# Kernel tuning notes

Measured on AMD Instinct MI355X. Metric: run time of the kernel, lower is better.

Reference implementation:

```python
import jax, jax.numpy as jnp
import numpy as np

D_MODEL = 512
N_HEADS = 16
D_HEAD = D_MODEL // N_HEADS


def _relative_shift(pos_score):
    # pos_score: [B, H, T, T]  (Transformer-XL shift trick)
    B, H, T1, T2 = pos_score.shape
    padded = jnp.pad(pos_score, ((0, 0), (0, 0), (0, 0), (1, 0)))  # [B,H,T1,T2+1]
    padded = padded.reshape(B, H, T2 + 1, T1)
    return padded[:, :, 1:].reshape(B, H, T1, T2)


def setup_inputs() -> dict:
    key = jax.random.key(0)
    ks = jax.random.split(key, 12)
    B, T, D = 4, 1024, D_MODEL
    s = 1.0 / np.sqrt(D)
    return {
        "q": jax.random.normal(ks[0], (B, T, D), jnp.float32),
        "k": jax.random.normal(ks[1], (B, T, D), jnp.float32),
        "v": jax.random.normal(ks[2], (B, T, D), jnp.float32),
        "pos_embedding": jax.random.normal(ks[3], (B, T, D), jnp.float32),
        "Wq": jax.random.normal(ks[4], (D, D), jnp.float32) * s,
        "bq": jnp.zeros((D,), jnp.float32),
        "Wp": jax.random.normal(ks[5], (D, D), jnp.float32) * s,
        "Wf": jax.random.normal(ks[6], (D, D), jnp.float32) * s,
        "bf": jnp.zeros((D,), jnp.float32),
        "u_bias": jax.random.normal(ks[7], (N_HEADS, D_HEAD), jnp.float32) * s,
        "v_bias": jax.random.normal(ks[8], (N_HEADS, D_HEAD), jnp.float32) * s,
    }


def reference(q, k, v, pos_embedding, Wq, bq, Wp, Wf, bf, u_bias, v_bias):
    B, T, D = q.shape
    H, Dh = N_HEADS, D_HEAD
    sqrt_dim = jnp.asarray(np.sqrt(D_MODEL), q.dtype)
    # NOTE: original module uses linear_q for q, k AND v (faithful to source)
    qh = (q @ Wq + bq).reshape(B, T, H, Dh)            # [B,T,H,Dh]
    kh = (k @ Wq + bq).reshape(B, T, H, Dh)
    vh = (v @ Wq + bq).reshape(B, T, H, Dh)
    ph = (pos_embedding @ Wp).reshape(B, T, H, Dh)     # no bias

    content_score = jnp.einsum('bthd,bshd->bhts', qh + u_bias, kh)
    pos_score = jnp.einsum('bthd,bshd->bhts', qh + v_bias, ph)
    pos_score = _relative_shift(pos_score)

    score = (content_score + pos_score) / sqrt_dim     # [B,H,T,T]
    attn = jax.nn.softmax(score, axis=-1)              # dropout identity in eval
    context = jnp.einsum('bhts,bshd->bthd', attn, vh).reshape(B, T, D)
    return context @ Wf + bf
```

## Files before the change

### kernel.cpp

```cpp
#include <hip/hip_runtime.h>
#include <hip/hip_bf16.h>

typedef __bf16 bf16;
typedef bf16 bf16x8 __attribute__((ext_vector_type(8)));
typedef bf16 bf16x4 __attribute__((ext_vector_type(4)));
typedef float f32x4 __attribute__((ext_vector_type(4)));

#define SCALE_LOG2 0.06376237f


__global__ __launch_bounds__(256) void prep_kernel(
    const float* __restrict__ Wq, const float* __restrict__ Wp, const float* __restrict__ Wf,
    bf16* __restrict__ WqT, bf16* __restrict__ WpT, bf16* __restrict__ WfT)
{
  const int tid = threadIdx.x;
  __shared__ bf16 t[64][72];
  const int m = blockIdx.x >> 6;
  const int tb = blockIdx.x & 63;
  const int tr = tb >> 3, tc = tb & 7;
  const float* W = (m == 0) ? Wq : (m == 1) ? Wp : Wf;
  bf16*        O = (m == 0) ? WqT : (m == 1) ? WpT : WfT;
  const int r = tid >> 2, cg = tid & 3;
  {
    const float* src = W + (size_t)(tr * 64 + r) * 512 + tc * 64 + cg * 16;
    f32x4 a = *(const f32x4*)src, b2 = *(const f32x4*)(src + 4);
    f32x4 c = *(const f32x4*)(src + 8), d = *(const f32x4*)(src + 12);
    bf16x8 lo, hi;
#pragma unroll
    for (int j = 0; j < 4; j++) { lo[j] = (bf16)a[j]; lo[4 + j] = (bf16)b2[j]; hi[j] = (bf16)c[j]; hi[4 + j] = (bf16)d[j]; }
    *(bf16x8*)(&t[r][cg * 16])     = lo;
    *(bf16x8*)(&t[r][cg * 16 + 8]) = hi;
  }
  __syncthreads();
  bf16x8 o0, o1;
#pragma unroll
  for (int j = 0; j < 8; j++) { o0[j] = t[cg * 16 + j][r]; o1[j] = t[cg * 16 + 8 + j][r]; }
  bf16* dst = O + (size_t)(tc * 64 + r) * 512 + tr * 64 + cg * 16;
  *(bf16x8*)dst = o0;
  *(bf16x8*)(dst + 8) = o1;
}

__global__ __launch_bounds__(256) void proj_gemm(
    const float* __restrict__ q, const float* __restrict__ k, const float* __restrict__ v,
    const float* __restrict__ pos,
    const bf16* __restrict__ WqT, const bf16* __restrict__ WpT, const float* __restrict__ bq,
    bf16* __restrict__ qh, bf16* __restrict__ kh, bf16* __restrict__ vT, bf16* __restrict__ phx)
{
  __shared__ float Asf[128 * 68];
  __shared__ bf16  Bs[128 * 72];
  const int tid = threadIdx.x;
  const int wave = tid >> 6, lane = tid & 63, quad = lane >> 4, ln = lane & 15;
  const int tn = blockIdx.x & 3;
  const int tm = blockIdx.x >> 2;
  const int kind = tm >> 5;
  const int rr0 = (tm & 31) * 128;
  const float* X = (kind == 0) ? q : (kind == 1) ? k : (kind == 2) ? v : pos;
  const bf16* WT = ((kind < 3) ? WqT : WpT) + (size_t)tn * 128 * 512;
  const int qn_ = (wave & 1) * 64;
  const int qr_ = (wave >> 1) * 64;
  const int srow = tid >> 2, scg = tid & 3;

  f32x4 acc[4][4] = {};

  for (int kk = 0; kk < 8; kk++) {
    const int k0 = kk * 64;
    {
      const float* p0 = X + (size_t)(rr0 + srow) * 512 + k0 + scg * 16;
      const float* p1 = X + (size_t)(rr0 + srow + 64) * 512 + k0 + scg * 16;
#pragma unroll
      for (int u = 0; u < 4; u++) {
        *(f32x4*)(Asf + srow * 68 + scg * 16 + u * 4)        = *(const f32x4*)(p0 + u * 4);
        *(f32x4*)(Asf + (srow + 64) * 68 + scg * 16 + u * 4) = *(const f32x4*)(p1 + u * 4);
      }
      const bf16* w0 = WT + (size_t)srow * 512 + k0 + scg * 16;
      const bf16* w1 = WT + (size_t)(srow + 64) * 512 + k0 + scg * 16;
      *(bf16x8*)(Bs + srow * 72 + scg * 16)            = *(const bf16x8*)w0;
      *(bf16x8*)(Bs + srow * 72 + scg * 16 + 8)        = *(const bf16x8*)(w0 + 8);
      *(bf16x8*)(Bs + (srow + 64) * 72 + scg * 16)     = *(const bf16x8*)w1;
      *(bf16x8*)(Bs + (srow + 64) * 72 + scg * 16 + 8) = *(const bf16x8*)(w1 + 8);
    }
    __syncthreads();
#pragma unroll
    for (int ks = 0; ks < 2; ks++) {
      bf16x8 wf[4], xf[4];
#pragma unroll
      for (int i = 0; i < 4; i++) {
        wf[i] = *(const bf16x8*)(Bs + (qn_ + i * 16 + ln) * 72 + ks * 32 + quad * 8);
        f32x4 lo = *(const f32x4*)(Asf + (qr_ + i * 16 + ln) * 68 + ks * 32 + quad * 8);
        f32x4 hi = *(const f32x4*)(Asf + (qr_ + i * 16 + ln) * 68 + ks * 32 + quad * 8 + 4);
        bf16x8 t;
#pragma unroll
        for (int j = 0; j < 4; j++) { t[j] = (bf16)lo[j]; t[4 + j] = (bf16)hi[j]; }
        xf[i] = t;
      }
#pragma unroll
      for (int i = 0; i < 4; i++)
#pragma unroll
        for (int j = 0; j < 4; j++)
          acc[i][j] = __builtin_amdgcn_mfma_f32_16x16x32_bf16(wf[i], xf[j], acc[i][j], 0, 0, 0);
    }
    __syncthreads();
  }

#pragma unroll
  for (int i = 0; i < 4; i++) {
    const int nn0 = tn * 128 + qn_ + i * 16 + quad * 4;
    const int dd0 = nn0 & 31, hh = nn0 >> 5;
    f32x4 b4 = {0.f, 0.f, 0.f, 0.f};
    if (kind < 3) b4 = *(const f32x4*)(bq + nn0);
#pragma unroll
    for (int j = 0; j < 4; j++) {
      const int rr = rr0 + qr_ + j * 16 + ln;
      const int bb = rr >> 10, tt = rr & 1023;
      const size_t base = (size_t)(bb * 16 + hh);
      bf16x4 pk;
#pragma unroll
      for (int r = 0; r < 4; r++) pk[r] = (bf16)(acc[i][j][r] + b4[r]);
      if (kind == 0)      *(bf16x4*)(qh + (base * 1024 + tt) * 32 + dd0) = pk;
      else if (kind == 1) *(bf16x4*)(kh + (base * 1024 + tt) * 32 + dd0) = pk;
      else if (kind == 2) {
#pragma unroll
        for (int r = 0; r < 4; r++) vT[(base * 32 + dd0 + r) * 1024 + tt] = pk[r];
      } else {
        *(bf16x4*)(phx + (base * 2048 + tt) * 32 + dd0) = pk;
        if (tt <= 1021) *(bf16x4*)(phx + (base * 2048 + tt + 1025) * 32 + dd0) = pk;
        if (tt == 1023) {
          bf16x4 zz = {};
          *(bf16x4*)(phx + (base * 2048 + 1024) * 32 + dd0) = zz;
          *(bf16x4*)(phx + (base * 2048 + 2047) * 32 + dd0) = zz;
        }
      }
    }
  }
}

__global__ __launch_bounds__(256, 4) void attn_kernel(
    const bf16* __restrict__ qh, const bf16* __restrict__ kh,
    const bf16* __restrict__ vT, const bf16* __restrict__ phx,
    const float* __restrict__ u_bias, const float* __restrict__ v_bias,
    bf16* __restrict__ ctx)
{
  __shared__ float fs[4 * 16 * 84];
  __shared__ bf16  pb[4 * 16 * 72];

  const int tid = threadIdx.x;
  const int wave = tid >> 6, lane = tid & 63, quad = lane >> 4, ln = lane & 15;
  const int wg = blockIdx.x;
  const int bh = wg & 63, tq = wg >> 6;
  const int h = bh & 15, b = bh >> 4;
  const int t0 = tq * 64;
  const bf16* qh_h  = qh  + (size_t)bh * 1024 * 32;
  const bf16* kh_h  = kh  + (size_t)bh * 1024 * 32;
  const bf16* vT_h  = vT  + (size_t)bh * 32 * 1024;
  const bf16* phx_h = phx + (size_t)bh * 2048 * 32;

  float* fsw = fs + wave * 16 * 84;
  bf16*  pbw = pb + wave * 16 * 72;

  bf16x8 qu, qva, qvn;
  {
    const int t = t0 + wave * 16 + ln;
    bf16x8 q0 = *(const bf16x8*)(qh_h + (size_t)t * 32 + quad * 8);
    bf16x8 q1 = *(const bf16x8*)(qh_h + (size_t)(t + 1) * 32 + quad * 8);
    const float* ubp = u_bias + h * 32 + quad * 8;
    const float* vbp = v_bias + h * 32 + quad * 8;
#pragma unroll
    for (int j = 0; j < 8; j++) {
      qu[j]  = (bf16)(((float)q0[j] + ubp[j]) * SCALE_LOG2);
      qva[j] = (bf16)(((float)q0[j] + vbp[j]) * SCALE_LOG2);
      qvn[j] = (bf16)(((float)q1[j] + vbp[j]) * SCALE_LOG2);
    }
  }

  f32x4 O0 = {0.f, 0.f, 0.f, 0.f}, O1 = {0.f, 0.f, 0.f, 0.f};
  float l_lane = 0.0f;
  const f32x4 zf = {0.f, 0.f, 0.f, 0.f};

#pragma unroll 2
  for (int si = 0; si < 16; si++) {
    const int s0 = si * 64;
    const int jb0 = s0 - t0 + 960 + (3 - wave) * 16;

#pragma unroll
    for (int i = 0; i < 5; i++) {
      bf16x8 pbf = *(const bf16x8*)(phx_h + (size_t)(jb0 + i * 16 + ln) * 32 + quad * 8);
      bf16x8 bsel = (jb0 + i * 16 >= 1024) ? qvn : qva;
      f32x4 f = __builtin_amdgcn_mfma_f32_16x16x32_bf16(pbf, bsel, zf, 0, 0, 0);
      *(f32x4*)(fsw + ln * 84 + i * 16 + quad * 4) = f;
    }

    f32x4 c[4];
#pragma unroll
    for (int cs = 0; cs < 4; cs++) {
      bf16x8 kbf = *(const bf16x8*)(kh_h + (size_t)(s0 + cs * 16 + ln) * 32 + quad * 8);
      c[cs] = __builtin_amdgcn_mfma_f32_16x16x32_bf16(kbf, qu, zf, 0, 0, 0);
    }

#pragma unroll
    for (int cs = 0; cs < 4; cs++) {
      bf16x4 pk;
#pragma unroll
      for (int r = 0; r < 4; r++) {
        const int col = cs * 16 + quad * 4 + r - ln + 15;
        const float p = exp2f(c[cs][r] + fsw[ln * 84 + col]);
        l_lane += p;
        pk[r] = (bf16)p;
      }
      *(bf16x4*)(pbw + ln * 72 + cs * 16 + quad * 4) = pk;
    }

#pragma unroll
    for (int kb = 0; kb < 2; kb++) {
      bf16x8 a  = *(const bf16x8*)(pbw + ln * 72 + kb * 32 + quad * 8);
      bf16x8 b0 = *(const bf16x8*)(vT_h + (size_t)ln * 1024 + s0 + kb * 32 + quad * 8);
      bf16x8 b1 = *(const bf16x8*)(vT_h + (size_t)(16 + ln) * 1024 + s0 + kb * 32 + quad * 8);
      O0 = __builtin_amdgcn_mfma_f32_16x16x32_bf16(a, b0, O0, 0, 0, 0);
      O1 = __builtin_amdgcn_mfma_f32_16x16x32_bf16(a, b1, O1, 0, 0, 0);
    }
  }

  l_lane += __shfl_xor(l_lane, 16);
  l_lane += __shfl_xor(l_lane, 32);
#pragma unroll
  for (int r = 0; r < 4; r++) {
    const float lr = __shfl(l_lane, quad * 4 + r);
    const float inv = 1.0f / lr;
    const int t = t0 + wave * 16 + quad * 4 + r;
    const size_t o = ((size_t)(b * 1024 + t)) * 512 + h * 32;
    ctx[o + ln]      = (bf16)(O0[r] * inv);
    ctx[o + 16 + ln] = (bf16)(O1[r] * inv);
  }
}

__global__ __launch_bounds__(256) void out_gemm(
    const bf16* __restrict__ ctx, const bf16* __restrict__ WfT, const float* __restrict__ bfv,
    float* __restrict__ out)
{
  __shared__ bf16 As[64 * 40];
  __shared__ bf16 Bs[128 * 40];
  const int tid = threadIdx.x;
  const int wave = tid >> 6, lane = tid & 63, quad = lane >> 4, ln = lane & 15;
  const int tn = blockIdx.x & 3;
  const int tm = blockIdx.x >> 2;
  const int rr0 = tm * 64;
  const bf16* WT = WfT + (size_t)tn * 128 * 512;
  const int qm = (wave & 1) * 32, qn = (wave >> 1) * 64;
  const int srow = tid >> 2, scg = tid & 3;

  f32x4 acc[2][4] = {};
  for (int kk = 0; kk < 16; kk++) {
    const int k0 = kk * 32;
    *(bf16x8*)(As + srow * 40 + scg * 8)        = *(const bf16x8*)(ctx + (size_t)(rr0 + srow) * 512 + k0 + scg * 8);
    *(bf16x8*)(Bs + srow * 40 + scg * 8)        = *(const bf16x8*)(WT + (size_t)srow * 512 + k0 + scg * 8);
    *(bf16x8*)(Bs + (srow + 64) * 40 + scg * 8) = *(const bf16x8*)(WT + (size_t)(srow + 64) * 512 + k0 + scg * 8);
    __syncthreads();
    bf16x8 af[2], bfm[4];
#pragma unroll
    for (int i = 0; i < 2; i++)
      af[i] = *(const bf16x8*)(As + (qm + i * 16 + ln) * 40 + quad * 8);
#pragma unroll
    for (int j = 0; j < 4; j++)
      bfm[j] = *(const bf16x8*)(Bs + (qn + j * 16 + ln) * 40 + quad * 8);
#pragma unroll
    for (int i = 0; i < 2; i++)
#pragma unroll
      for (int j = 0; j < 4; j++)
        acc[i][j] = __builtin_amdgcn_mfma_f32_16x16x32_bf16(af[i], bfm[j], acc[i][j], 0, 0, 0);
    __syncthreads();
  }

#pragma unroll
  for (int i = 0; i < 2; i++)
#pragma unroll
    for (int j = 0; j < 4; j++) {
      const int nn = tn * 128 + qn + j * 16 + ln;
      const float bias = bfv[nn];
#pragma unroll
      for (int r = 0; r < 4; r++) {
        const int rr = rr0 + qm + i * 16 + quad * 4 + r;
        out[(size_t)rr * 512 + nn] = acc[i][j][r] + bias;
      }
    }
}

extern "C" void kernel_launch(void* const* d_in, const int* in_sizes, int n_in,
                              void* d_out, int out_size, void* d_ws, size_t ws_size,
                              hipStream_t stream) {
  const float* q   = (const float*)d_in[0];
  const float* k   = (const float*)d_in[1];
  const float* v   = (const float*)d_in[2];
  const float* pe  = (const float*)d_in[3];
  const float* Wq  = (const float*)d_in[4];
  const float* bq  = (const float*)d_in[5];
  const float* Wp  = (const float*)d_in[6];
  const float* Wf  = (const float*)d_in[7];
  const float* bfv = (const float*)d_in[8];
  const float* ub  = (const float*)d_in[9];
  const float* vb  = (const float*)d_in[10];

  bf16* ws  = (bf16*)d_ws;
  bf16* qh  = ws;
  bf16* kh  = qh + 2097152;
  bf16* vT  = kh + 2097152;
  bf16* phx = vT + 2097152;
  bf16* ctx = phx + 4194304;
  bf16* WqT = ctx + 2097152;
  bf16* WpT = WqT + 262144;
  bf16* WfT = WpT + 262144;

  prep_kernel<<<192, 256, 0, stream>>>(Wq, Wp, Wf, WqT, WpT, WfT);
  proj_gemm<<<512, 256, 0, stream>>>(q, k, v, pe, WqT, WpT, bq, qh, kh, vT, phx);
  attn_kernel<<<1024, 256, 0, stream>>>(qh, kh, vT, phx, ub, vb, ctx);
  out_gemm<<<256, 256, 0, stream>>>(ctx, WfT, bfv, (float*)d_out);
}
```

Before: 190.4 us.

## Split attention over key halves with combine kernel and shrink projection tiles

The attention kernel now runs 2-wave blocks over 32 query rows and splits the key range into two halves. Each half writes unnormalized bf16 partial outputs and row sums, and a new combine kernel adds them and divides by the total. The projection GEMM uses 64-row tiles, doubling its grid, and the attention kernel shares one LDS buffer for scores and probabilities. The goal is more parallelism and occupancy on a large-CU GPU, at the cost of an extra kernel launch, extra global traffic for the partials, and bf16 rounding of unnormalized partials. Because there is no running max in the softmax, the two halves combine correctly without rescaling.

```diff
diff --git a/kernel.cpp b/kernel.cpp
--- a/kernel.cpp
+++ b/kernel.cpp
@@ -46,57 +46,55 @@
     const bf16* __restrict__ WqT, const bf16* __restrict__ WpT, const float* __restrict__ bq,
     bf16* __restrict__ qh, bf16* __restrict__ kh, bf16* __restrict__ vT, bf16* __restrict__ phx)
 {
-  __shared__ float Asf[128 * 68];
+  __shared__ float Asf[64 * 68];
   __shared__ bf16  Bs[128 * 72];
   const int tid = threadIdx.x;
   const int wave = tid >> 6, lane = tid & 63, quad = lane >> 4, ln = lane & 15;
   const int tn = blockIdx.x & 3;
   const int tm = blockIdx.x >> 2;
-  const int kind = tm >> 5;
-  const int rr0 = (tm & 31) * 128;
+  const int kind = tm >> 6;
+  const int rr0 = (tm & 63) * 64;
   const float* X = (kind == 0) ? q : (kind == 1) ? k : (kind == 2) ? v : pos;
   const bf16* WT = ((kind < 3) ? WqT : WpT) + (size_t)tn * 128 * 512;
-  const int qn_ = (wave & 1) * 64;
-  const int qr_ = (wave >> 1) * 64;
-  const int srow = tid >> 2, scg = tid & 3;
-
-  f32x4 acc[4][4] = {};
+  const int qn_ = (wave >> 1) * 64;
+  const int qr_ = (wave & 1) * 32;
+  const int arow = tid >> 2, acg = tid & 3;
+  const int brow = tid >> 1, bcg = tid & 1;
+
+  f32x4 acc[4][2] = {};
 
   for (int kk = 0; kk < 8; kk++) {
     const int k0 = kk * 64;
     {
-      const float* p0 = X + (size_t)(rr0 + srow) * 512 + k0 + scg * 16;
-      const float* p1 = X + (size_t)(rr0 + srow + 64) * 512 + k0 + scg * 16;
-#pragma unroll
-      for (int u = 0; u < 4; u++) {
-        *(f32x4*)(Asf + srow * 68 + scg * 16 + u * 4)        = *(const f32x4*)(p0 + u * 4);
-        *(f32x4*)(Asf + (srow + 64) * 68 + scg * 16 + u * 4) = *(const f32x4*)(p1 + u * 4);
-      }
-      const bf16* w0 = WT + (size_t)srow * 512 + k0 + scg * 16;
-      const bf16* w1 = WT + (size_t)(srow + 64) * 512 + k0 + scg * 16;
-      *(bf16x8*)(Bs + srow * 72 + scg * 16)            = *(const bf16x8*)w0;
-      *(bf16x8*)(Bs + srow * 72 + scg * 16 + 8)        = *(const bf16x8*)(w0 + 8);
-      *(bf16x8*)(Bs + (srow + 64) * 72 + scg * 16)     = *(const bf16x8*)w1;
-      *(bf16x8*)(Bs + (srow + 64) * 72 + scg * 16 + 8) = *(const bf16x8*)(w1 + 8);
+      const float* p0 = X + (size_t)(rr0 + arow) * 512 + k0 + acg * 16;
+#pragma unroll
+      for (int u = 0; u < 4; u++)
+        *(f32x4*)(Asf + arow * 68 + acg * 16 + u * 4) = *(const f32x4*)(p0 + u * 4);
+      const bf16* w0 = WT + (size_t)brow * 512 + k0 + bcg * 32;
+#pragma unroll
+      for (int u = 0; u < 4; u++)
+        *(bf16x8*)(Bs + brow * 72 + bcg * 32 + u * 8) = *(const bf16x8*)(w0 + u * 8);
     }
     __syncthreads();
 #pragma unroll
     for (int ks = 0; ks < 2; ks++) {
-      bf16x8 wf[4], xf[4];
-#pragma unroll
-      for (int i = 0; i < 4; i++) {
+      bf16x8 wf[4], xf[2];
+#pragma unroll
+      for (int i = 0; i < 4; i++)
         wf[i] = *(const bf16x8*)(Bs + (qn_ + i * 16 + ln) * 72 + ks * 32 + quad * 8);
-        f32x4 lo = *(const f32x4*)(Asf + (qr_ + i * 16 + ln) * 68 + ks * 32 + quad * 8);
-        f32x4 hi = *(const f32x4*)(Asf + (qr_ + i * 16 + ln) * 68 + ks * 32 + quad * 8 + 4);
+#pragma unroll
+      for (int j = 0; j < 2; j++) {
+        f32x4 lo = *(const f32x4*)(Asf + (qr_ + j * 16 + ln) * 68 + ks * 32 + quad * 8);
+        f32x4 hi = *(const f32x4*)(Asf + (qr_ + j * 16 + ln) * 68 + ks * 32 + quad * 8 + 4);
         bf16x8 t;
 #pragma unroll
-        for (int j = 0; j < 4; j++) { t[j] = (bf16)lo[j]; t[4 + j] = (bf16)hi[j]; }
-        xf[i] = t;
+        for (int u = 0; u < 4; u++) { t[u] = (bf16)lo[u]; t[4 + u] = (bf16)hi[u]; }
+        xf[j] = t;
       }
 #pragma unroll
       for (int i = 0; i < 4; i++)
 #pragma unroll
-        for (int j = 0; j < 4; j++)
+        for (int j = 0; j < 2; j++)
           acc[i][j] = __builtin_amdgcn_mfma_f32_16x16x32_bf16(wf[i], xf[j], acc[i][j], 0, 0, 0);
     }
     __syncthreads();
@@ -109,7 +107,7 @@
     f32x4 b4 = {0.f, 0.f, 0.f, 0.f};
     if (kind < 3) b4 = *(const f32x4*)(bq + nn0);
 #pragma unroll
-    for (int j = 0; j < 4; j++) {
+    for (int j = 0; j < 2; j++) {
       const int rr = rr0 + qr_ + j * 16 + ln;
       const int bb = rr >> 10, tt = rr & 1023;
       const size_t base = (size_t)(bb * 16 + hh);
@@ -134,32 +132,33 @@
   }
 }
 
-__global__ __launch_bounds__(256, 4) void attn_kernel(
+__global__ __launch_bounds__(128, 8) void attn_kernel(
     const bf16* __restrict__ qh, const bf16* __restrict__ kh,
     const bf16* __restrict__ vT, const bf16* __restrict__ phx,
     const float* __restrict__ u_bias, const float* __restrict__ v_bias,
-    bf16* __restrict__ ctx)
-{
-  __shared__ float fs[4 * 16 * 84];
-  __shared__ bf16  pb[4 * 16 * 72];
+    bf16* __restrict__ partO, float* __restrict__ partL)
+{
+  __shared__ float fs2[2 * 16 * 82];
 
   const int tid = threadIdx.x;
   const int wave = tid >> 6, lane = tid & 63, quad = lane >> 4, ln = lane & 15;
   const int wg = blockIdx.x;
-  const int bh = wg & 63, tq = wg >> 6;
+  const int bh = wg & 63;
+  const int rest = wg >> 6;
+  const int tt32 = rest & 31, half = rest >> 5;
   const int h = bh & 15, b = bh >> 4;
-  const int t0 = tq * 64;
+  const int t0w = tt32 * 32 + wave * 16;
   const bf16* qh_h  = qh  + (size_t)bh * 1024 * 32;
   const bf16* kh_h  = kh  + (size_t)bh * 1024 * 32;
   const bf16* vT_h  = vT  + (size_t)bh * 32 * 1024;
   const bf16* phx_h = phx + (size_t)bh * 2048 * 32;
 
-  float* fsw = fs + wave * 16 * 84;
-  bf16*  pbw = pb + wave * 16 * 72;
+  float* fsw = fs2 + wave * 16 * 82;
+  bf16*  pbw = (bf16*)fsw;
 
   bf16x8 qu, qva, qvn;
   {
-    const int t = t0 + wave * 16 + ln;
+    const int t = t0w + ln;
     bf16x8 q0 = *(const bf16x8*)(qh_h + (size_t)t * 32 + quad * 8);
     bf16x8 q1 = *(const bf16x8*)(qh_h + (size_t)(t + 1) * 32 + quad * 8);
     const float* ubp = u_bias + h * 32 + quad * 8;
@@ -176,17 +175,16 @@
   float l_lane = 0.0f;
   const f32x4 zf = {0.f, 0.f, 0.f, 0.f};
 
-#pragma unroll 2
-  for (int si = 0; si < 16; si++) {
+  for (int si = half * 8; si < half * 8 + 8; si++) {
     const int s0 = si * 64;
-    const int jb0 = s0 - t0 + 960 + (3 - wave) * 16;
+    const int jb0 = s0 - t0w + 1008;
 
 #pragma unroll
     for (int i = 0; i < 5; i++) {
       bf16x8 pbf = *(const bf16x8*)(phx_h + (size_t)(jb0 + i * 16 + ln) * 32 + quad * 8);
       bf16x8 bsel = (jb0 + i * 16 >= 1024) ? qvn : qva;
       f32x4 f = __builtin_amdgcn_mfma_f32_16x16x32_bf16(pbf, bsel, zf, 0, 0, 0);
-      *(f32x4*)(fsw + ln * 84 + i * 16 + quad * 4) = f;
+      *(f32x4*)(fsw + ln * 82 + i * 16 + quad * 4) = f;
     }
 
     f32x4 c[4];
@@ -196,22 +194,30 @@
       c[cs] = __builtin_amdgcn_mfma_f32_16x16x32_bf16(kbf, qu, zf, 0, 0, 0);
     }
 
+    float sc_[4][4];
+#pragma unroll
+    for (int cs = 0; cs < 4; cs++)
+#pragma unroll
+      for (int r = 0; r < 4; r++) {
+        const int col = cs * 16 + quad * 4 + r - ln + 15;
+        sc_[cs][r] = c[cs][r] + fsw[ln * 82 + col];
+      }
+
 #pragma unroll
     for (int cs = 0; cs < 4; cs++) {
       bf16x4 pk;
 #pragma unroll
       for (int r = 0; r < 4; r++) {
-        const int col = cs * 16 + quad * 4 + r - ln + 15;
-        const float p = exp2f(c[cs][r] + fsw[ln * 84 + col]);
+        const float p = exp2f(sc_[cs][r]);
         l_lane += p;
         pk[r] = (bf16)p;
       }
-      *(bf16x4*)(pbw + ln * 72 + cs * 16 + quad * 4) = pk;
+      *(bf16x4*)(pbw + ln * 76 + cs * 16 + quad * 4) = pk;
     }
 
 #pragma unroll
     for (int kb = 0; kb < 2; kb++) {
-      bf16x8 a  = *(const bf16x8*)(pbw + ln * 72 + kb * 32 + quad * 8);
+      bf16x8 a  = *(const bf16x8*)(pbw + ln * 76 + kb * 32 + quad * 8);
       bf16x8 b0 = *(const bf16x8*)(vT_h + (size_t)ln * 1024 + s0 + kb * 32 + quad * 8);
       bf16x8 b1 = *(const bf16x8*)(vT_h + (size_t)(16 + ln) * 1024 + s0 + kb * 32 + quad * 8);
       O0 = __builtin_amdgcn_mfma_f32_16x16x32_bf16(a, b0, O0, 0, 0, 0);
@@ -221,15 +227,31 @@
 
   l_lane += __shfl_xor(l_lane, 16);
   l_lane += __shfl_xor(l_lane, 32);
+  if (quad == 0) partL[wg * 32 + wave * 16 + ln] = l_lane;
 #pragma unroll
   for (int r = 0; r < 4; r++) {
-    const float lr = __shfl(l_lane, quad * 4 + r);
-    const float inv = 1.0f / lr;
-    const int t = t0 + wave * 16 + quad * 4 + r;
-    const size_t o = ((size_t)(b * 1024 + t)) * 512 + h * 32;
-    ctx[o + ln]      = (bf16)(O0[r] * inv);
-    ctx[o + 16 + ln] = (bf16)(O1[r] * inv);
-  }
+    const size_t pbase = (size_t)wg * 1024 + (wave * 16 + quad * 4 + r) * 32;
+    partO[pbase + ln]      = (bf16)O0[r];
+    partO[pbase + 16 + ln] = (bf16)O1[r];
+  }
+}
+
+__global__ __launch_bounds__(256) void combine_kernel(
+    const bf16* __restrict__ partO, const float* __restrict__ partL, bf16* __restrict__ ctx)
+{
+  const int idx = blockIdx.x * 256 + threadIdx.x;
+  const int c = idx & 511;
+  const int t = (idx >> 9) & 1023;
+  const int b = idx >> 19;
+  const int h = c >> 5, d = c & 31;
+  const int bh = b * 16 + h;
+  const int wgA = bh + 64 * (t >> 5);
+  const int wgB = wgA + 64 * 32;
+  const int row = t & 31;
+  const float a  = (float)partO[(size_t)wgA * 1024 + row * 32 + d];
+  const float b2 = (float)partO[(size_t)wgB * 1024 + row * 32 + d];
+  const float l  = partL[wgA * 32 + row] + partL[wgB * 32 + row];
+  ctx[idx] = (bf16)((a + b2) / l);
 }
 
 __global__ __launch_bounds__(256) void out_gemm(
@@ -307,9 +329,12 @@
   bf16* WqT = ctx + 2097152;
   bf16* WpT = WqT + 262144;
   bf16* WfT = WpT + 262144;
+  bf16*  partO = WfT + 262144;
+  float* partL = (float*)(partO + 4194304);
 
   prep_kernel<<<192, 256, 0, stream>>>(Wq, Wp, Wf, WqT, WpT, WfT);
-  proj_gemm<<<512, 256, 0, stream>>>(q, k, v, pe, WqT, WpT, bq, qh, kh, vT, phx);
-  attn_kernel<<<1024, 256, 0, stream>>>(qh, kh, vT, phx, ub, vb, ctx);
+  proj_gemm<<<1024, 256, 0, stream>>>(q, k, v, pe, WqT, WpT, bq, qh, kh, vT, phx);
+  attn_kernel<<<4096, 128, 0, stream>>>(qh, kh, vT, phx, ub, vb, partO, partL);
+  combine_kernel<<<8192, 256, 0, stream>>>(partO, partL, ctx);
   out_gemm<<<256, 256, 0, stream>>>(ctx, WfT, bfv, (float*)d_out);
 }
```

Result: slower. 224.3 us (+17.8%).

## Rewrite projection and output GEMMs as LDS-free small-tile direct-load kernels

Applied to the files above, without the earlier changes.

Both the input projection GEMM and the output GEMM drop shared-memory staging and barriers. Each wave now loads its operand fragments straight from global memory into MFMA registers, working on a 16-row by 64-column tile, and the grid grows to 2048 and 512 workgroups. The goal is to remove LDS round-trips and __syncthreads stalls, raise occupancy and spread the work over more CUs. The cost is less data reuse: X rows are reloaded by every column wave and weights are read by many more workgroups, so global and L2 traffic rise. The fp32 activation loads are also uncoalesced 32-byte strided chunks.

```diff
diff --git a/kernel.cpp b/kernel.cpp
--- a/kernel.cpp
+++ b/kernel.cpp
@@ -40,95 +40,65 @@
   *(bf16x8*)(dst + 8) = o1;
 }
 
-__global__ __launch_bounds__(256) void proj_gemm(
+__global__ __launch_bounds__(256, 8) void proj_gemm(
     const float* __restrict__ q, const float* __restrict__ k, const float* __restrict__ v,
     const float* __restrict__ pos,
     const bf16* __restrict__ WqT, const bf16* __restrict__ WpT, const float* __restrict__ bq,
     bf16* __restrict__ qh, bf16* __restrict__ kh, bf16* __restrict__ vT, bf16* __restrict__ phx)
 {
-  __shared__ float Asf[128 * 68];
-  __shared__ bf16  Bs[128 * 72];
   const int tid = threadIdx.x;
   const int wave = tid >> 6, lane = tid & 63, quad = lane >> 4, ln = lane & 15;
-  const int tn = blockIdx.x & 3;
-  const int tm = blockIdx.x >> 2;
-  const int kind = tm >> 5;
-  const int rr0 = (tm & 31) * 128;
+  const int wg = blockIdx.x;
+  const int rr_glob = wg >> 1;
+  const int kind = rr_glob >> 8;
+  const int rr0 = (rr_glob & 255) * 16;
+  const int nn0 = ((wg & 1) * 4 + wave) * 64;
   const float* X = (kind == 0) ? q : (kind == 1) ? k : (kind == 2) ? v : pos;
-  const bf16* WT = ((kind < 3) ? WqT : WpT) + (size_t)tn * 128 * 512;
-  const int qn_ = (wave & 1) * 64;
-  const int qr_ = (wave >> 1) * 64;
-  const int srow = tid >> 2, scg = tid & 3;
-
-  f32x4 acc[4][4] = {};
-
-  for (int kk = 0; kk < 8; kk++) {
-    const int k0 = kk * 64;
-    {
-      const float* p0 = X + (size_t)(rr0 + srow) * 512 + k0 + scg * 16;
-      const float* p1 = X + (size_t)(rr0 + srow + 64) * 512 + k0 + scg * 16;
-#pragma unroll
-      for (int u = 0; u < 4; u++) {
-        *(f32x4*)(Asf + srow * 68 + scg * 16 + u * 4)        = *(const f32x4*)(p0 + u * 4);
-        *(f32x4*)(Asf + (srow + 64) * 68 + scg * 16 + u * 4) = *(const f32x4*)(p1 + u * 4);
-      }
-      const bf16* w0 = WT + (size_t)srow * 512 + k0 + scg * 16;
-      const bf16* w1 = WT + (size_t)(srow + 64) * 512 + k0 + scg * 16;
-      *(bf16x8*)(Bs + srow * 72 + scg * 16)            = *(const bf16x8*)w0;
-      *(bf16x8*)(Bs + srow * 72 + scg * 16 + 8)        = *(const bf16x8*)(w0 + 8);
-      *(bf16x8*)(Bs + (srow + 64) * 72 + scg * 16)     = *(const bf16x8*)w1;
-      *(bf16x8*)(Bs + (srow + 64) * 72 + scg * 16 + 8) = *(const bf16x8*)(w1 + 8);
-    }
-    __syncthreads();
-#pragma unroll
-    for (int ks = 0; ks < 2; ks++) {
-      bf16x8 wf[4], xf[4];
-#pragma unroll
-      for (int i = 0; i < 4; i++) {
-        wf[i] = *(const bf16x8*)(Bs + (qn_ + i * 16 + ln) * 72 + ks * 32 + quad * 8);
-        f32x4 lo = *(const f32x4*)(Asf + (qr_ + i * 16 + ln) * 68 + ks * 32 + quad * 8);
-        f32x4 hi = *(const f32x4*)(Asf + (qr_ + i * 16 + ln) * 68 + ks * 32 + quad * 8 + 4);
-        bf16x8 t;
-#pragma unroll
-        for (int j = 0; j < 4; j++) { t[j] = (bf16)lo[j]; t[4 + j] = (bf16)hi[j]; }
-        xf[i] = t;
-      }
-#pragma unroll
-      for (int i = 0; i < 4; i++)
-#pragma unroll
-        for (int j = 0; j < 4; j++)
-          acc[i][j] = __builtin_amdgcn_mfma_f32_16x16x32_bf16(wf[i], xf[j], acc[i][j], 0, 0, 0);
-    }
-    __syncthreads();
-  }
-
+  const bf16* WT = (kind < 3) ? WqT : WpT;
+
+  f32x4 acc[4] = {};
+
+  const float* xp = X + (size_t)(rr0 + ln) * 512 + quad * 8;
+  const bf16*  wp = WT + (size_t)(nn0 + ln) * 512 + quad * 8;
+#pragma unroll 4
+  for (int ks = 0; ks < 16; ks++) {
+    const int k0 = ks * 32;
+    f32x4 lo = *(const f32x4*)(xp + k0);
+    f32x4 hi = *(const f32x4*)(xp + k0 + 4);
+    bf16x8 xf;
+#pragma unroll
+    for (int j = 0; j < 4; j++) { xf[j] = (bf16)lo[j]; xf[4 + j] = (bf16)hi[j]; }
+#pragma unroll
+    for (int i = 0; i < 4; i++) {
+      bf16x8 wf = *(const bf16x8*)(wp + (size_t)i * 16 * 512 + k0);
+      acc[i] = __builtin_amdgcn_mfma_f32_16x16x32_bf16(wf, xf, acc[i], 0, 0, 0);
+    }
+  }
+
+  const int rr = rr0 + ln;
+  const int bb = rr >> 10, tt = rr & 1023;
 #pragma unroll
   for (int i = 0; i < 4; i++) {
-    const int nn0 = tn * 128 + qn_ + i * 16 + quad * 4;
-    const int dd0 = nn0 & 31, hh = nn0 >> 5;
+    const int nnb = nn0 + i * 16 + quad * 4;
+    const int dd0 = nnb & 31, hh = nnb >> 5;
+    const size_t base = (size_t)(bb * 16 + hh);
     f32x4 b4 = {0.f, 0.f, 0.f, 0.f};
-    if (kind < 3) b4 = *(const f32x4*)(bq + nn0);
-#pragma unroll
-    for (int j = 0; j < 4; j++) {
-      const int rr = rr0 + qr_ + j * 16 + ln;
-      const int bb = rr >> 10, tt = rr & 1023;
-      const size_t base = (size_t)(bb * 16 + hh);
-      bf16x4 pk;
-#pragma unroll
-      for (int r = 0; r < 4; r++) pk[r] = (bf16)(acc[i][j][r] + b4[r]);
-      if (kind == 0)      *(bf16x4*)(qh + (base * 1024 + tt) * 32 + dd0) = pk;
-      else if (kind == 1) *(bf16x4*)(kh + (base * 1024 + tt) * 32 + dd0) = pk;
-      else if (kind == 2) {
-#pragma unroll
-        for (int r = 0; r < 4; r++) vT[(base * 32 + dd0 + r) * 1024 + tt] = pk[r];
-      } else {
-        *(bf16x4*)(phx + (base * 2048 + tt) * 32 + dd0) = pk;
-        if (tt <= 1021) *(bf16x4*)(phx + (base * 2048 + tt + 1025) * 32 + dd0) = pk;
-        if (tt == 1023) {
-          bf16x4 zz = {};
-          *(bf16x4*)(phx + (base * 2048 + 1024) * 32 + dd0) = zz;
-          *(bf16x4*)(phx + (base * 2048 + 2047) * 32 + dd0) = zz;
-        }
+    if (kind < 3) b4 = *(const f32x4*)(bq + nnb);
+    bf16x4 pk;
+#pragma unroll
+    for (int r = 0; r < 4; r++) pk[r] = (bf16)(acc[i][r] + b4[r]);
+    if (kind == 0)      *(bf16x4*)(qh + (base * 1024 + tt) * 32 + dd0) = pk;
+    else if (kind == 1) *(bf16x4*)(kh + (base * 1024 + tt) * 32 + dd0) = pk;
+    else if (kind == 2) {
+#pragma unroll
+      for (int r = 0; r < 4; r++) vT[(base * 32 + dd0 + r) * 1024 + tt] = pk[r];
+    } else {
+      *(bf16x4*)(phx + (base * 2048 + tt) * 32 + dd0) = pk;
+      if (tt <= 1021) *(bf16x4*)(phx + (base * 2048 + tt + 1025) * 32 + dd0) = pk;
+      if (tt == 1023) {
+        bf16x4 zz = {};
+        *(bf16x4*)(phx + (base * 2048 + 1024) * 32 + dd0) = zz;
+        *(bf16x4*)(phx + (base * 2048 + 2047) * 32 + dd0) = zz;
       }
     }
   }
@@ -232,55 +202,40 @@
   }
 }
 
-__global__ __launch_bounds__(256) void out_gemm(
+__global__ __launch_bounds__(256, 8) void out_gemm(
     const bf16* __restrict__ ctx, const bf16* __restrict__ WfT, const float* __restrict__ bfv,
     float* __restrict__ out)
 {
-  __shared__ bf16 As[64 * 40];
-  __shared__ bf16 Bs[128 * 40];
   const int tid = threadIdx.x;
   const int wave = tid >> 6, lane = tid & 63, quad = lane >> 4, ln = lane & 15;
-  const int tn = blockIdx.x & 3;
-  const int tm = blockIdx.x >> 2;
-  const int rr0 = tm * 64;
-  const bf16* WT = WfT + (size_t)tn * 128 * 512;
-  const int qm = (wave & 1) * 32, qn = (wave >> 1) * 64;
-  const int srow = tid >> 2, scg = tid & 3;
-
-  f32x4 acc[2][4] = {};
-  for (int kk = 0; kk < 16; kk++) {
-    const int k0 = kk * 32;
-    *(bf16x8*)(As + srow * 40 + scg * 8)        = *(const bf16x8*)(ctx + (size_t)(rr0 + srow) * 512 + k0 + scg * 8);
-    *(bf16x8*)(Bs + srow * 40 + scg * 8)        = *(const bf16x8*)(WT + (size_t)srow * 512 + k0 + scg * 8);
-    *(bf16x8*)(Bs + (srow + 64) * 40 + scg * 8) = *(const bf16x8*)(WT + (size_t)(srow + 64) * 512 + k0 + scg * 8);
-    __syncthreads();
-    bf16x8 af[2], bfm[4];
-#pragma unroll
-    for (int i = 0; i < 2; i++)
-      af[i] = *(const bf16x8*)(As + (qm + i * 16 + ln) * 40 + quad * 8);
-#pragma unroll
-    for (int j = 0; j < 4; j++)
-      bfm[j] = *(const bf16x8*)(Bs + (qn + j * 16 + ln) * 40 + quad * 8);
-#pragma unroll
-    for (int i = 0; i < 2; i++)
-#pragma unroll
-      for (int j = 0; j < 4; j++)
-        acc[i][j] = __builtin_amdgcn_mfma_f32_16x16x32_bf16(af[i], bfm[j], acc[i][j], 0, 0, 0);
-    __syncthreads();
-  }
-
-#pragma unroll
-  for (int i = 0; i < 2; i++)
-#pragma unroll
-    for (int j = 0; j < 4; j++) {
-      const int nn = tn * 128 + qn + j * 16 + ln;
-      const float bias = bfv[nn];
-#pragma unroll
-      for (int r = 0; r < 4; r++) {
-        const int rr = rr0 + qm + i * 16 + quad * 4 + r;
-        out[(size_t)rr * 512 + nn] = acc[i][j][r] + bias;
-      }
-    }
+  const int wg = blockIdx.x;
+  const int rr0 = (wg >> 1) * 16;
+  const int nn0 = ((wg & 1) * 4 + wave) * 64;
+
+  f32x4 acc[4] = {};
+  const bf16* cp = ctx + (size_t)(rr0 + ln) * 512 + quad * 8;
+  const bf16* wp = WfT + (size_t)(nn0 + ln) * 512 + quad * 8;
+#pragma unroll 4
+  for (int ks = 0; ks < 16; ks++) {
+    const int k0 = ks * 32;
+    bf16x8 cf = *(const bf16x8*)(cp + k0);
+#pragma unroll
+    for (int i = 0; i < 4; i++) {
+      bf16x8 wf = *(const bf16x8*)(wp + (size_t)i * 16 * 512 + k0);
+      acc[i] = __builtin_amdgcn_mfma_f32_16x16x32_bf16(wf, cf, acc[i], 0, 0, 0);
+    }
+  }
+
+  const int rr = rr0 + ln;
+#pragma unroll
+  for (int i = 0; i < 4; i++) {
+    const int nnb = nn0 + i * 16 + quad * 4;
+    f32x4 b4 = *(const f32x4*)(bfv + nnb);
+    f32x4 o;
+#pragma unroll
+    for (int r = 0; r < 4; r++) o[r] = acc[i][r] + b4[r];
+    *(f32x4*)(out + (size_t)rr * 512 + nnb) = o;
+  }
 }
 
 extern "C" void kernel_launch(void* const* d_in, const int* in_sizes, int n_in,
@@ -309,7 +264,7 @@
   bf16* WfT = WpT + 262144;
 
   prep_kernel<<<192, 256, 0, stream>>>(Wq, Wp, Wf, WqT, WpT, WfT);
-  proj_gemm<<<512, 256, 0, stream>>>(q, k, v, pe, WqT, WpT, bq, qh, kh, vT, phx);
+  proj_gemm<<<2048, 256, 0, stream>>>(q, k, v, pe, WqT, WpT, bq, qh, kh, vT, phx);
   attn_kernel<<<1024, 256, 0, stream>>>(qh, kh, vT, phx, ub, vb, ctx);
-  out_gemm<<<256, 256, 0, stream>>>(ctx, WfT, bfv, (float*)d_out);
-}
+  out_gemm<<<512, 256, 0, stream>>>(ctx, WfT, bfv, (float*)d_out);
+}
```

Result: slower. 263.0 us (+38.1%).
